# Performance work log

Hardware: AMD Instinct MI355X
Metric: run time of the kernel (lower is better)

## Reference

```python
import jax, jax.numpy as jnp
import numpy as np

EMBED = 1024
DSTATE = 16
DCONV = 4
DTRANK = 64  # ceil(EMBED/16)
B = 2
T = 2048


def setup_inputs() -> dict:
    key = jax.random.key(0)
    ks = jax.random.split(key, 8)
    def w(k, shape, s=0.02):
        return jax.random.normal(k, shape, dtype=jnp.float32) * s
    return dict(
        x=jax.random.normal(ks[0], (B, T, EMBED), dtype=jnp.float32),
        in_proj_w=w(ks[1], (2 * EMBED, EMBED)), in_proj_b=jnp.zeros((2 * EMBED,), jnp.float32),
        conv_w=w(ks[2], (EMBED, 1, DCONV)), conv_b=jnp.zeros((EMBED,), jnp.float32),
        x_proj_w=w(ks[3], (DTRANK + 2 * DSTATE, EMBED)), x_proj_b=jnp.zeros((DTRANK + 2 * DSTATE,), jnp.float32),
        dt_proj_w=w(ks[4], (EMBED, DTRANK)), dt_proj_b=jnp.zeros((EMBED,), jnp.float32),
        A_log=jnp.log(jnp.arange(1, DSTATE + 1, dtype=jnp.float32))[None, :],  # (1,N) as in torch module
        D_param=jnp.ones((EMBED,), jnp.float32),
        out_proj_w=w(ks[5], (EMBED, EMBED)), out_proj_b=jnp.zeros((EMBED,), jnp.float32),
        skip_proj_w=w(ks[6], (EMBED, EMBED)), skip_proj_b=jnp.zeros((EMBED,), jnp.float32),
    )


def reference(x, in_proj_w, in_proj_b, conv_w, conv_b, x_proj_w, x_proj_b,
              dt_proj_w, dt_proj_b, A_log, D_param, out_proj_w, out_proj_b,
              skip_proj_w, skip_proj_b):
    Bsz, Tlen, Dm = x.shape
    # in_proj and split into ssm branch and gate branch
    xr = x @ in_proj_w.T + in_proj_b            # (B,T,2D)
    x_in, res = jnp.split(xr, 2, axis=-1)
    # depthwise causal conv1d (torch pads both sides then slices [:T] == left-pad)
    xc = jax.lax.conv_general_dilated(
        x_in.transpose(0, 2, 1), conv_w, (1,), [(DCONV - 1, 0)],
        dimension_numbers=('NCH', 'OIH', 'NCH'), feature_group_count=Dm)
    xc = (xc + conv_b[None, :, None]).transpose(0, 2, 1)  # (B,T,D)
    xc = jax.nn.silu(xc)
    # input-dependent SSM params
    ssm = xc @ x_proj_w.T + x_proj_b            # (B,T,dt_rank+2N)
    delta, Bp, Cp = jnp.split(ssm, [DTRANK, DTRANK + DSTATE], axis=-1)
    delta = jax.nn.softplus(delta @ dt_proj_w.T + dt_proj_b)  # (B,T,D)
    A = -jnp.exp(A_log)                          # (1,N)
    dA = jnp.exp(delta[..., None] * A)           # (B,T,D,N)
    dBu = delta[..., None] * Bp[:, :, None, :] * xc[..., None]  # (B,T,D,N)
    # inclusive associative scan over time: h_t = dA_t * h_{t-1} + dBu_t
    def op(l, r):
        Ai, Bi = l
        Aj, Bj = r
        return (Aj * Ai, Bj + Aj * Bi)
    _, ys = jax.lax.associative_scan(op, (dA, dBu), axis=1)
    y = (ys * Cp[:, :, None, :]).sum(-1)         # (B,T,D)
    y = y + xc * D_param
    y = y * jax.nn.silu(res)
    return y @ out_proj_w.T + out_proj_b + (x @ skip_proj_w.T + skip_proj_b)
```

## Files before the change

kernel.cpp:

```cpp
#include <hip/hip_runtime.h>
#include <math.h>

#define EMBED  1024
#define DSTATE 16
#define DCONV  4
#define DTRANK 64
#define BB     2
#define TT     2048
#define M_TOK  (BB*TT)
#define SSMW   96
#define NCHUNK 64
#define CLEN   (TT/NCHUNK)
#define KSPLIT 8

typedef __attribute__((ext_vector_type(8))) __bf16 bf16x8;
typedef __attribute__((ext_vector_type(4))) float floatx4;

__device__ __forceinline__ float silu_f(float x) {
    return x / (1.0f + __expf(-x));
}
__device__ __forceinline__ float softplus_f(float x) {
    return fmaxf(x, 0.0f) + log1pf(__expf(-fabsf(x)));
}
__device__ __forceinline__ unsigned short f2bf(float f) {
    union { float f; unsigned int u; } v; v.f = f;
    unsigned int u = v.u;
    return (unsigned short)((u + 0x7fffu + ((u >> 16) & 1u)) >> 16);
}
__device__ __forceinline__ float bf2f(unsigned short s) {
    union { unsigned int u; float f; } v; v.u = ((unsigned int)s) << 16;
    return v.f;
}
__device__ __forceinline__ void async16(unsigned short* lds, const unsigned short* g) {
    __builtin_amdgcn_global_load_lds(
        (const __attribute__((address_space(1))) unsigned int*)g,
        (__attribute__((address_space(3))) unsigned int*)lds, 16, 0, 0);
}

#define GEMM_DECODE \
    const int tid = threadIdx.x; const int wid = tid >> 6; \
    const int lane = tid & 63; \
    const int wm = wid >> 1, wn = wid & 1; \
    const int lr = lane & 15; const int lq = lane >> 4;

__device__ __forceinline__ void gemm_acc(
    const unsigned short* __restrict__ A, int lda,
    const unsigned short* __restrict__ W, int ldw,
    int m0, int n0, int k0, int klen, floatx4 (&acc)[4][4])
{
    __shared__ unsigned short As[128 * 32];
    __shared__ unsigned short Ws[128 * 32];
    GEMM_DECODE;
    const int l0 = tid,       row0 = l0 >> 2;
    const int l1 = tid + 256, row1 = l1 >> 2;
    const int kc0 = (((l0 & 3) ^ ((row0 >> 1) & 3)) * 8);
    const int kc1 = (((l1 & 3) ^ ((row1 >> 1) & 3)) * 8);

    for (int kt = k0; kt < k0 + klen; kt += 32) {
        async16(&As[l0 * 8], A + (size_t)(m0 + row0) * lda + kt + kc0);
        async16(&As[l1 * 8], A + (size_t)(m0 + row1) * lda + kt + kc1);
        async16(&Ws[l0 * 8], W + (size_t)(n0 + row0) * ldw + kt + kc0);
        async16(&Ws[l1 * 8], W + (size_t)(n0 + row1) * ldw + kt + kc1);
        __syncthreads();

        bf16x8 af[4], bfr[4];
        #pragma unroll
        for (int i = 0; i < 4; ++i) {
            int ra = wm * 64 + i * 16 + lr;
            af[i] = *(const bf16x8*)&As[ra * 32 + ((lq ^ ((ra >> 1) & 3)) * 8)];
        }
        #pragma unroll
        for (int i = 0; i < 4; ++i) {
            int rb = wn * 64 + i * 16 + lr;
            bfr[i] = *(const bf16x8*)&Ws[rb * 32 + ((lq ^ ((rb >> 1) & 3)) * 8)];
        }

        #pragma unroll
        for (int mi = 0; mi < 4; ++mi)
            #pragma unroll
            for (int ni = 0; ni < 4; ++ni)
                acc[mi][ni] = __builtin_amdgcn_mfma_f32_16x16x32_bf16(
                    af[mi], bfr[ni], acc[mi][ni], 0, 0, 0);
        __syncthreads();
    }
}

__global__ __launch_bounds__(256)
void gemm_in(const unsigned short* __restrict__ A,
             const unsigned short* __restrict__ W,
             const float* __restrict__ bias,
             unsigned short* __restrict__ xrb, unsigned short* __restrict__ gate)
{
    floatx4 acc[4][4] = {};
    const int m0 = blockIdx.x * 128, n0 = blockIdx.y * 128;
    gemm_acc(A, 2 * EMBED, W, EMBED, m0, n0, 0, EMBED, acc);
    GEMM_DECODE;
    #pragma unroll
    for (int mi = 0; mi < 4; ++mi)
        #pragma unroll
        for (int ni = 0; ni < 4; ++ni) {
            int nb = n0 + wn * 64 + ni * 16 + lr;
            #pragma unroll
            for (int r = 0; r < 4; ++r) {
                int m = m0 + wm * 64 + mi * 16 + lq * 4 + r;
                float v = acc[mi][ni][r] + bias[nb];
                if (nb < EMBED) xrb[(size_t)m * EMBED + nb] = f2bf(v);
                else gate[(size_t)m * EMBED + nb - EMBED] = f2bf(silu_f(v));
            }
        }
}

__global__ __launch_bounds__(256)
void gemm_xp(const unsigned short* __restrict__ A,
             const unsigned short* __restrict__ W,
             float* __restrict__ xpart)
{
    floatx4 acc[4][4] = {};
    const int m0 = blockIdx.x * 128;
    const int k0 = blockIdx.z * (EMBED / KSPLIT);
    gemm_acc(A, EMBED, W, EMBED, m0, 0, k0, EMBED / KSPLIT, acc);
    GEMM_DECODE;
    float* base = xpart + (size_t)blockIdx.z * M_TOK * SSMW;
    #pragma unroll
    for (int mi = 0; mi < 4; ++mi)
        #pragma unroll
        for (int ni = 0; ni < 4; ++ni) {
            int nb = wn * 64 + ni * 16 + lr;
            if (nb < SSMW) {
                #pragma unroll
                for (int r = 0; r < 4; ++r) {
                    int m = m0 + wm * 64 + mi * 16 + lq * 4 + r;
                    base[(size_t)m * SSMW + nb] = acc[mi][ni][r];
                }
            }
        }
}

__global__ __launch_bounds__(256)
void xp_merge(const float* __restrict__ xpart, const float* __restrict__ xp_b,
              float* __restrict__ ssm, unsigned short* __restrict__ dtin)
{
    int idx = blockIdx.x * 256 + threadIdx.x;
    if (idx >= M_TOK * SSMW) return;
    int m = idx / SSMW, n = idx - m * SSMW;
    float s = xp_b[n];
    #pragma unroll
    for (int z = 0; z < KSPLIT; ++z) s += xpart[(size_t)z * M_TOK * SSMW + idx];
    ssm[idx] = s;
    if (n < DTRANK) dtin[(size_t)m * DTRANK + n] = f2bf(s);
}

__global__ __launch_bounds__(256)
void gemm_dt(const unsigned short* __restrict__ A,
             const unsigned short* __restrict__ W,
             const float* __restrict__ bias,
             unsigned short* __restrict__ dltb)
{
    floatx4 acc[4][4] = {};
    const int m0 = blockIdx.x * 128, n0 = blockIdx.y * 128;
    gemm_acc(A, DTRANK, W, DTRANK, m0, n0, 0, DTRANK, acc);
    GEMM_DECODE;
    #pragma unroll
    for (int mi = 0; mi < 4; ++mi)
        #pragma unroll
        for (int ni = 0; ni < 4; ++ni) {
            int nb = n0 + wn * 64 + ni * 16 + lr;
            #pragma unroll
            for (int r = 0; r < 4; ++r) {
                int m = m0 + wm * 64 + mi * 16 + lq * 4 + r;
                dltb[(size_t)m * EMBED + nb] = f2bf(softplus_f(acc[mi][ni][r] + bias[nb]));
            }
        }
}

__global__ __launch_bounds__(256)
void gemm_out(const unsigned short* __restrict__ A,
              const unsigned short* __restrict__ W,
              const float* __restrict__ bias, const float* __restrict__ bias2,
              float* __restrict__ C)
{
    floatx4 acc[4][4] = {};
    const int m0 = blockIdx.x * 128, n0 = blockIdx.y * 128;
    gemm_acc(A, 2 * EMBED, W, 2 * EMBED, m0, n0, 0, 2 * EMBED, acc);
    GEMM_DECODE;
    #pragma unroll
    for (int mi = 0; mi < 4; ++mi)
        #pragma unroll
        for (int ni = 0; ni < 4; ++ni) {
            int nb = n0 + wn * 64 + ni * 16 + lr;
            float bb = bias[nb] + bias2[nb];
            #pragma unroll
            for (int r = 0; r < 4; ++r) {
                int m = m0 + wm * 64 + mi * 16 + lq * 4 + r;
                C[(size_t)m * EMBED + nb] = acc[mi][ni][r] + bb;
            }
        }
}

#define SEG0 524288
#define SEG1 (SEG0 + 16384)
#define SEG2 (SEG1 + 32768)
#define SEG3 (SEG2 + 524288)
#define SEG4 (SEG3 + 1048576)

__global__ __launch_bounds__(256)
void cvt_pack(const float* __restrict__ in_w, const float* __restrict__ dt_w,
              const float* __restrict__ xp_w, const float* __restrict__ ow,
              const float* __restrict__ sw, const float* __restrict__ x,
              unsigned short* __restrict__ inwb, unsigned short* __restrict__ dtwb,
              unsigned short* __restrict__ xpwb, unsigned short* __restrict__ wcat,
              unsigned short* __restrict__ Acat)
{
    int j = blockIdx.x * 256 + threadIdx.x;
    if (j >= SEG4) return;
    float4 v = {0.f, 0.f, 0.f, 0.f};
    unsigned short* dst;
    if (j < SEG0) {
        v = *(const float4*)&in_w[j * 4];
        dst = &inwb[j * 4];
    } else if (j < SEG1) {
        int i = (j - SEG0) * 4;
        v = *(const float4*)&dt_w[i];
        dst = &dtwb[i];
    } else if (j < SEG2) {
        int i = (j - SEG1) * 4;
        if ((i >> 10) < SSMW) v = *(const float4*)&xp_w[i];
        dst = &xpwb[i];
    } else if (j < SEG3) {
        int i = (j - SEG2) * 4;
        int n = i >> 11, k = i & 2047;
        v = *(const float4*)((k < EMBED) ? &ow[(size_t)n * EMBED + k]
                                         : &sw[(size_t)n * EMBED + (k - EMBED)]);
        dst = &wcat[i];
    } else {
        int i = (j - SEG3) * 4;
        int m = i >> 10, k = i & 1023;
        v = *(const float4*)&x[i];
        dst = &Acat[(size_t)m * 2 * EMBED + EMBED + k];
    }
    ushort4 o = { f2bf(v.x), f2bf(v.y), f2bf(v.z), f2bf(v.w) };
    *(ushort4*)dst = o;
}

__global__ __launch_bounds__(256)
void conv_silu(const unsigned short* __restrict__ xrb,
               const float* __restrict__ conv_w,
               const float* __restrict__ conv_b,
               unsigned short* __restrict__ xcb)
{
    int idx = blockIdx.x * 256 + threadIdx.x;
    if (idx >= BB * TT * EMBED / 4) return;
    int dq = idx & (EMBED / 4 - 1);
    int t  = (idx >> 8) & (TT - 1);
    int b  = idx >> 19;
    int d  = dq * 4;

    float4 cw0 = *(const float4*)&conv_w[(d + 0) * 4];
    float4 cw1 = *(const float4*)&conv_w[(d + 1) * 4];
    float4 cw2 = *(const float4*)&conv_w[(d + 2) * 4];
    float4 cw3 = *(const float4*)&conv_w[(d + 3) * 4];
    float4 s   = *(const float4*)&conv_b[d];

    const float* w0 = (const float*)&cw0;
    const float* w1 = (const float*)&cw1;
    const float* w2 = (const float*)&cw2;
    const float* w3 = (const float*)&cw3;

    #pragma unroll
    for (int jj = 0; jj < 4; ++jj) {
        int tr = t - 3 + jj;
        if (tr >= 0) {
            ushort4 u = *(const ushort4*)&xrb[(size_t)(b * TT + tr) * EMBED + d];
            s.x = fmaf(w0[jj], bf2f(u.x), s.x);
            s.y = fmaf(w1[jj], bf2f(u.y), s.y);
            s.z = fmaf(w2[jj], bf2f(u.z), s.z);
            s.w = fmaf(w3[jj], bf2f(u.w), s.w);
        }
    }
    ushort4 o = { f2bf(silu_f(s.x)), f2bf(silu_f(s.y)),
                  f2bf(silu_f(s.z)), f2bf(silu_f(s.w)) };
    *(ushort4*)&xcb[(size_t)(b * TT + t) * EMBED + d] = o;
}

__global__ __launch_bounds__(256)
void scan_chunk(const unsigned short* __restrict__ deltab,
                const unsigned short* __restrict__ xcb,
                const float* __restrict__ ssm,
                const float* __restrict__ A_log,
                float* __restrict__ hout,
                float* __restrict__ Ssum)
{
    __shared__ float Bs[CLEN][DSTATE];
    const int tid = threadIdx.x;
    const int blk = blockIdx.x;
    const int dg = blk & 3, chunk = (blk >> 2) & (NCHUNK - 1), b = blk >> 8;
    const int d = dg * 256 + tid;
    const int t0 = chunk * CLEN;

    for (int i = tid; i < CLEN * DSTATE; i += 256) {
        int t = i >> 4, n = i & 15;
        Bs[t][n] = ssm[(size_t)(b * TT + t0 + t) * SSMW + DTRANK + n];
    }
    __syncthreads();

    float An[DSTATE];
    #pragma unroll
    for (int n = 0; n < DSTATE; ++n) An[n] = -__expf(A_log[n]);

    float h[DSTATE] = {};
    float S = 0.f;
    for (int t = 0; t < CLEN; ++t) {
        size_t row = (size_t)(b * TT + t0 + t);
        float dv = bf2f(deltab[row * EMBED + d]);
        float xv = bf2f(xcb[row * EMBED + d]);
        S += dv;
        float sx = dv * xv;
        float Bv[DSTATE];
        *(float4*)&Bv[0]  = *(const float4*)&Bs[t][0];
        *(float4*)&Bv[4]  = *(const float4*)&Bs[t][4];
        *(float4*)&Bv[8]  = *(const float4*)&Bs[t][8];
        *(float4*)&Bv[12] = *(const float4*)&Bs[t][12];
        #pragma unroll
        for (int n = 0; n < DSTATE; ++n) {
            float dA = __expf(dv * An[n]);
            h[n] = fmaf(dA, h[n], sx * Bv[n]);
        }
    }
    size_t base = ((size_t)(chunk * BB + b) * EMBED + d) * DSTATE;
    #pragma unroll
    for (int jj = 0; jj < 4; ++jj)
        *(float4*)&hout[base + jj * 4] = *(float4*)&h[jj * 4];
    Ssum[(size_t)(chunk * BB + b) * EMBED + d] = S;
}

__global__ __launch_bounds__(256)
void scan_combine(const float* __restrict__ A_log,
                  const float* __restrict__ Ssum,
                  const float* __restrict__ hout,
                  float* __restrict__ hin)
{
    int idx = blockIdx.x * 256 + threadIdx.x;
    int n  = idx & 15;
    int bd = idx >> 4;
    float An = -__expf(A_log[n]);
    float h = 0.f;
    for (int c0 = 0; c0 < NCHUNK; c0 += 8) {
        float ho[8], S[8];
        #pragma unroll
        for (int jj = 0; jj < 8; ++jj) {
            ho[jj] = hout[(size_t)(c0 + jj) * (BB * EMBED * DSTATE) + idx];
            S[jj]  = Ssum[(size_t)(c0 + jj) * (BB * EMBED) + bd];
        }
        #pragma unroll
        for (int jj = 0; jj < 8; ++jj) {
            hin[(size_t)(c0 + jj) * (BB * EMBED * DSTATE) + idx] = h;
            h = fmaf(__expf(An * S[jj]), h, ho[jj]);
        }
    }
}

__global__ __launch_bounds__(256)
void scan_apply(const unsigned short* __restrict__ deltab,
                const unsigned short* __restrict__ xcb,
                const float* __restrict__ ssm,
                const float* __restrict__ A_log,
                const float* __restrict__ D_param,
                const unsigned short* __restrict__ gate,
                const float* __restrict__ hin,
                unsigned short* __restrict__ Acat)
{
    __shared__ float Bs[CLEN][DSTATE];
    __shared__ float Cs[CLEN][DSTATE];
    const int tid = threadIdx.x;
    const int blk = blockIdx.x;
    const int dg = blk & 3, chunk = (blk >> 2) & (NCHUNK - 1), b = blk >> 8;
    const int d = dg * 256 + tid;
    const int t0 = chunk * CLEN;

    for (int i = tid; i < CLEN * DSTATE; i += 256) {
        int t = i >> 4, n = i & 15;
        size_t row = (size_t)(b * TT + t0 + t);
        Bs[t][n] = ssm[row * SSMW + DTRANK + n];
        Cs[t][n] = ssm[row * SSMW + DTRANK + DSTATE + n];
    }
    __syncthreads();

    float An[DSTATE];
    #pragma unroll
    for (int n = 0; n < DSTATE; ++n) An[n] = -__expf(A_log[n]);
    float Dd = D_param[d];

    float h[DSTATE];
    size_t base = ((size_t)(chunk * BB + b) * EMBED + d) * DSTATE;
    #pragma unroll
    for (int jj = 0; jj < 4; ++jj)
        *(float4*)&h[jj * 4] = *(const float4*)&hin[base + jj * 4];

    for (int t = 0; t < CLEN; ++t) {
        size_t row = (size_t)(b * TT + t0 + t);
        float dv = bf2f(deltab[row * EMBED + d]);
        float xv = bf2f(xcb[row * EMBED + d]);
        float sx = dv * xv;
        float Bv[DSTATE], Cv[DSTATE];
        *(float4*)&Bv[0]  = *(const float4*)&Bs[t][0];
        *(float4*)&Bv[4]  = *(const float4*)&Bs[t][4];
        *(float4*)&Bv[8]  = *(const float4*)&Bs[t][8];
        *(float4*)&Bv[12] = *(const float4*)&Bs[t][12];
        *(float4*)&Cv[0]  = *(const float4*)&Cs[t][0];
        *(float4*)&Cv[4]  = *(const float4*)&Cs[t][4];
        *(float4*)&Cv[8]  = *(const float4*)&Cs[t][8];
        *(float4*)&Cv[12] = *(const float4*)&Cs[t][12];
        float y0 = 0.f, y1 = 0.f, y2 = 0.f, y3 = 0.f;
        #pragma unroll
        for (int n = 0; n < DSTATE; n += 4) {
            float dA0 = __expf(dv * An[n + 0]);
            float dA1 = __expf(dv * An[n + 1]);
            float dA2 = __expf(dv * An[n + 2]);
            float dA3 = __expf(dv * An[n + 3]);
            h[n + 0] = fmaf(dA0, h[n + 0], sx * Bv[n + 0]);
            h[n + 1] = fmaf(dA1, h[n + 1], sx * Bv[n + 1]);
            h[n + 2] = fmaf(dA2, h[n + 2], sx * Bv[n + 2]);
            h[n + 3] = fmaf(dA3, h[n + 3], sx * Bv[n + 3]);
            y0 = fmaf(h[n + 0], Cv[n + 0], y0);
            y1 = fmaf(h[n + 1], Cv[n + 1], y1);
            y2 = fmaf(h[n + 2], Cv[n + 2], y2);
            y3 = fmaf(h[n + 3], Cv[n + 3], y3);
        }
        float yv = (y0 + y1) + (y2 + y3) + xv * Dd;
        float g = bf2f(gate[row * EMBED + d]);
        Acat[row * 2 * EMBED + d] = f2bf(yv * g);
    }
}

extern "C" void kernel_launch(void* const* d_in, const int* in_sizes, int n_in,
                              void* d_out, int out_size, void* d_ws, size_t ws_size,
                              hipStream_t stream) {
    const float* x      = (const float*)d_in[0];
    const float* in_w   = (const float*)d_in[1];
    const float* in_b   = (const float*)d_in[2];
    const float* conv_w = (const float*)d_in[3];
    const float* conv_b = (const float*)d_in[4];
    const float* xp_w   = (const float*)d_in[5];
    const float* xp_b   = (const float*)d_in[6];
    const float* dt_w   = (const float*)d_in[7];
    const float* dt_b   = (const float*)d_in[8];
    const float* A_log  = (const float*)d_in[9];
    const float* Dp     = (const float*)d_in[10];
    const float* out_w  = (const float*)d_in[11];
    const float* out_b  = (const float*)d_in[12];
    const float* skip_w = (const float*)d_in[13];
    const float* skip_b = (const float*)d_in[14];
    float* out = (float*)d_out;

    float* ws    = (float*)d_ws;
    float* ssm   = ws;
    float* xpart = ssm   + (size_t)M_TOK * SSMW;
    float* hout  = xpart + (size_t)KSPLIT * M_TOK * SSMW;
    float* hin   = hout  + (size_t)NCHUNK * BB * EMBED * DSTATE;
    float* Ssum  = hin   + (size_t)NCHUNK * BB * EMBED * DSTATE;
    unsigned short* Acat = (unsigned short*)(Ssum + (size_t)NCHUNK * BB * EMBED);
    unsigned short* xrb  = Acat + (size_t)M_TOK * 2 * EMBED;
    unsigned short* xcb  = xrb  + (size_t)M_TOK * EMBED;
    unsigned short* dltb = xcb  + (size_t)M_TOK * EMBED;
    unsigned short* dtin = dltb + (size_t)M_TOK * EMBED;
    unsigned short* gate = dtin + (size_t)M_TOK * DTRANK;
    unsigned short* inwb = gate + (size_t)M_TOK * EMBED;
    unsigned short* xpwb = inwb + (size_t)2 * EMBED * EMBED;
    unsigned short* dtwb = xpwb + (size_t)128 * EMBED;
    unsigned short* wcat = dtwb + (size_t)EMBED * DTRANK;

    dim3 blk(256);

    cvt_pack<<<(SEG4 + 255) / 256, blk, 0, stream>>>(
        in_w, dt_w, xp_w, out_w, skip_w, x, inwb, dtwb, xpwb, wcat, Acat);

    gemm_in<<<dim3(M_TOK / 128, 2 * EMBED / 128), blk, 0, stream>>>(
        Acat + EMBED, inwb, in_b, xrb, gate);

    conv_silu<<<(M_TOK * EMBED / 4 + 255) / 256, blk, 0, stream>>>(
        xrb, conv_w, conv_b, xcb);

    gemm_xp<<<dim3(M_TOK / 128, 1, KSPLIT), blk, 0, stream>>>(xcb, xpwb, xpart);
    xp_merge<<<(M_TOK * SSMW + 255) / 256, blk, 0, stream>>>(xpart, xp_b, ssm, dtin);

    gemm_dt<<<dim3(M_TOK / 128, EMBED / 128), blk, 0, stream>>>(
        dtin, dtwb, dt_b, dltb);

    scan_chunk<<<BB * NCHUNK * (EMBED / 256), blk, 0, stream>>>(
        dltb, xcb, ssm, A_log, hout, Ssum);
    scan_combine<<<(BB * EMBED * DSTATE + 255) / 256, blk, 0, stream>>>(
        A_log, Ssum, hout, hin);
    scan_apply<<<BB * NCHUNK * (EMBED / 256), blk, 0, stream>>>(
        dltb, xcb, ssm, A_log, Dp, gate, hin, Acat);

    gemm_out<<<dim3(M_TOK / 128, EMBED / 128), blk, 0, stream>>>(
        Acat, wcat, out_b, skip_b, out);
}
```

Before: 319.4 us.

## Fold dt_proj into x_proj weights, replacing split-K xp GEMM and dt GEMM

Precomputes a fused weight W_dt·W_xp[:64] (plus the B/C rows of x_proj) in a small kernel, so one GEMM over K=1024 with N=1152 produces delta and B/C directly. This removes the split-K partial buffers, the merge kernel and the separate rank-64 GEMM with its bf16 round-trip. In exchange the delta GEMM grows from K=64 to K=1024 over 1024 outputs, and the rounding path changes. Softplus is also simplified to a threshold plus log(1+exp).

```diff
diff --git a/kernel.cpp b/kernel.cpp
--- a/kernel.cpp
+++ b/kernel.cpp
@@ -8,10 +8,9 @@
 #define BB     2
 #define TT     2048
 #define M_TOK  (BB*TT)
-#define SSMW   96
 #define NCHUNK 64
 #define CLEN   (TT/NCHUNK)
-#define KSPLIT 8
+#define NMID   1152
 
 typedef __attribute__((ext_vector_type(8))) __bf16 bf16x8;
 typedef __attribute__((ext_vector_type(4))) float floatx4;
@@ -20,7 +19,7 @@
     return x / (1.0f + __expf(-x));
 }
 __device__ __forceinline__ float softplus_f(float x) {
-    return fmaxf(x, 0.0f) + log1pf(__expf(-fabsf(x)));
+    return (x > 15.0f) ? x : __logf(1.0f + __expf(x));
 }
 __device__ __forceinline__ unsigned short f2bf(float f) {
     union { float f; unsigned int u; } v; v.f = f;
@@ -111,64 +110,64 @@
 }
 
 __global__ __launch_bounds__(256)
-void gemm_xp(const unsigned short* __restrict__ A,
-             const unsigned short* __restrict__ W,
-             float* __restrict__ xpart)
-{
-    floatx4 acc[4][4] = {};
-    const int m0 = blockIdx.x * 128;
-    const int k0 = blockIdx.z * (EMBED / KSPLIT);
-    gemm_acc(A, EMBED, W, EMBED, m0, 0, k0, EMBED / KSPLIT, acc);
-    GEMM_DECODE;
-    float* base = xpart + (size_t)blockIdx.z * M_TOK * SSMW;
-    #pragma unroll
-    for (int mi = 0; mi < 4; ++mi)
-        #pragma unroll
-        for (int ni = 0; ni < 4; ++ni) {
-            int nb = wn * 64 + ni * 16 + lr;
-            if (nb < SSMW) {
-                #pragma unroll
-                for (int r = 0; r < 4; ++r) {
-                    int m = m0 + wm * 64 + mi * 16 + lq * 4 + r;
-                    base[(size_t)m * SSMW + nb] = acc[mi][ni][r];
-                }
-            }
-        }
-}
-
-__global__ __launch_bounds__(256)
-void xp_merge(const float* __restrict__ xpart, const float* __restrict__ xp_b,
-              float* __restrict__ ssm, unsigned short* __restrict__ dtin)
-{
-    int idx = blockIdx.x * 256 + threadIdx.x;
-    if (idx >= M_TOK * SSMW) return;
-    int m = idx / SSMW, n = idx - m * SSMW;
-    float s = xp_b[n];
-    #pragma unroll
-    for (int z = 0; z < KSPLIT; ++z) s += xpart[(size_t)z * M_TOK * SSMW + idx];
-    ssm[idx] = s;
-    if (n < DTRANK) dtin[(size_t)m * DTRANK + n] = f2bf(s);
-}
-
-__global__ __launch_bounds__(256)
-void gemm_dt(const unsigned short* __restrict__ A,
-             const unsigned short* __restrict__ W,
-             const float* __restrict__ bias,
-             unsigned short* __restrict__ dltb)
+void wfuse_kernel(const float* __restrict__ dt_w, const float* __restrict__ xp_w,
+                  const float* __restrict__ xp_b, const float* __restrict__ dt_b,
+                  unsigned short* __restrict__ wmid, float* __restrict__ bias_mid)
+{
+    __shared__ float dtl[4][64];
+    const int t = threadIdx.x;
+    dtl[t >> 6][t & 63] = dt_w[(size_t)(blockIdx.x * 4 + (t >> 6)) * DTRANK + (t & 63)];
+    __syncthreads();
+    const int dloc = t >> 6, kq = t & 63;
+    const int d = blockIdx.x * 4 + dloc;
+
+    #pragma unroll
+    for (int j = 0; j < 4; ++j) {
+        float4 acc = {0.f, 0.f, 0.f, 0.f};
+        const int kb = j * 256 + kq * 4;
+        for (int r = 0; r < 64; ++r) {
+            float4 xv = *(const float4*)&xp_w[(size_t)r * EMBED + kb];
+            float s = dtl[dloc][r];
+            acc.x = fmaf(s, xv.x, acc.x);
+            acc.y = fmaf(s, xv.y, acc.y);
+            acc.z = fmaf(s, xv.z, acc.z);
+            acc.w = fmaf(s, xv.w, acc.w);
+        }
+        ushort4 o = { f2bf(acc.x), f2bf(acc.y), f2bf(acc.z), f2bf(acc.w) };
+        *(ushort4*)&wmid[(size_t)d * EMBED + kb] = o;
+    }
+
+    if (kq == 0) {
+        float b = dt_b[d];
+        for (int r = 0; r < 64; ++r) b = fmaf(dtl[dloc][r], xp_b[r], b);
+        bias_mid[d] = b;
+    }
+    if (blockIdx.x == 0 && t < 128)
+        bias_mid[1024 + t] = (t < 32) ? xp_b[DTRANK + t] : 0.f;
+}
+
+__global__ __launch_bounds__(256)
+void gemm_mid(const unsigned short* __restrict__ A,
+              const unsigned short* __restrict__ W,
+              const float* __restrict__ bias_mid,
+              unsigned short* __restrict__ dltb, float* __restrict__ bc)
 {
     floatx4 acc[4][4] = {};
     const int m0 = blockIdx.x * 128, n0 = blockIdx.y * 128;
-    gemm_acc(A, DTRANK, W, DTRANK, m0, n0, 0, DTRANK, acc);
+    gemm_acc(A, EMBED, W, EMBED, m0, n0, 0, EMBED, acc);
     GEMM_DECODE;
     #pragma unroll
     for (int mi = 0; mi < 4; ++mi)
         #pragma unroll
         for (int ni = 0; ni < 4; ++ni) {
             int nb = n0 + wn * 64 + ni * 16 + lr;
+            float bb = bias_mid[nb];
             #pragma unroll
             for (int r = 0; r < 4; ++r) {
                 int m = m0 + wm * 64 + mi * 16 + lq * 4 + r;
-                dltb[(size_t)m * EMBED + nb] = f2bf(softplus_f(acc[mi][ni][r] + bias[nb]));
+                float v = acc[mi][ni][r] + bb;
+                if (nb < 1024) dltb[(size_t)m * EMBED + nb] = f2bf(softplus_f(v));
+                else if (nb < 1056) bc[(size_t)m * 32 + nb - 1024] = v;
             }
         }
 }
@@ -197,46 +196,41 @@
         }
 }
 
-#define SEG0 524288
-#define SEG1 (SEG0 + 16384)
-#define SEG2 (SEG1 + 32768)
-#define SEG3 (SEG2 + 524288)
-#define SEG4 (SEG3 + 1048576)
-
-__global__ __launch_bounds__(256)
-void cvt_pack(const float* __restrict__ in_w, const float* __restrict__ dt_w,
-              const float* __restrict__ xp_w, const float* __restrict__ ow,
-              const float* __restrict__ sw, const float* __restrict__ x,
-              unsigned short* __restrict__ inwb, unsigned short* __restrict__ dtwb,
-              unsigned short* __restrict__ xpwb, unsigned short* __restrict__ wcat,
-              unsigned short* __restrict__ Acat)
+#define SA 524288
+#define SB (SA + 524288)
+#define SC (SB + 1048576)
+#define SD (SC + 32768)
+
+__global__ __launch_bounds__(256)
+void cvt_pack(const float* __restrict__ in_w, const float* __restrict__ xp_w,
+              const float* __restrict__ ow, const float* __restrict__ sw,
+              const float* __restrict__ x,
+              unsigned short* __restrict__ inwb, unsigned short* __restrict__ wcat,
+              unsigned short* __restrict__ Acat, unsigned short* __restrict__ wmid)
 {
     int j = blockIdx.x * 256 + threadIdx.x;
-    if (j >= SEG4) return;
+    if (j >= SD) return;
     float4 v = {0.f, 0.f, 0.f, 0.f};
     unsigned short* dst;
-    if (j < SEG0) {
+    if (j < SA) {
         v = *(const float4*)&in_w[j * 4];
         dst = &inwb[j * 4];
-    } else if (j < SEG1) {
-        int i = (j - SEG0) * 4;
-        v = *(const float4*)&dt_w[i];
-        dst = &dtwb[i];
-    } else if (j < SEG2) {
-        int i = (j - SEG1) * 4;
-        if ((i >> 10) < SSMW) v = *(const float4*)&xp_w[i];
-        dst = &xpwb[i];
-    } else if (j < SEG3) {
-        int i = (j - SEG2) * 4;
+    } else if (j < SB) {
+        int i = (j - SA) * 4;
         int n = i >> 11, k = i & 2047;
         v = *(const float4*)((k < EMBED) ? &ow[(size_t)n * EMBED + k]
                                          : &sw[(size_t)n * EMBED + (k - EMBED)]);
         dst = &wcat[i];
-    } else {
-        int i = (j - SEG3) * 4;
+    } else if (j < SC) {
+        int i = (j - SB) * 4;
         int m = i >> 10, k = i & 1023;
         v = *(const float4*)&x[i];
         dst = &Acat[(size_t)m * 2 * EMBED + EMBED + k];
+    } else {
+        int i = (j - SC) * 4;
+        int row = i >> 10, k = i & 1023;
+        if (row < 32) v = *(const float4*)&xp_w[(size_t)(DTRANK + row) * EMBED + k];
+        dst = &wmid[(size_t)(1024 + row) * EMBED + k];
     }
     ushort4 o = { f2bf(v.x), f2bf(v.y), f2bf(v.z), f2bf(v.w) };
     *(ushort4*)dst = o;
@@ -285,7 +279,7 @@
 __global__ __launch_bounds__(256)
 void scan_chunk(const unsigned short* __restrict__ deltab,
                 const unsigned short* __restrict__ xcb,
-                const float* __restrict__ ssm,
+                const float* __restrict__ bc,
                 const float* __restrict__ A_log,
                 float* __restrict__ hout,
                 float* __restrict__ Ssum)
@@ -299,7 +293,7 @@
 
     for (int i = tid; i < CLEN * DSTATE; i += 256) {
         int t = i >> 4, n = i & 15;
-        Bs[t][n] = ssm[(size_t)(b * TT + t0 + t) * SSMW + DTRANK + n];
+        Bs[t][n] = bc[(size_t)(b * TT + t0 + t) * 32 + n];
     }
     __syncthreads();
 
@@ -362,7 +356,7 @@
 __global__ __launch_bounds__(256)
 void scan_apply(const unsigned short* __restrict__ deltab,
                 const unsigned short* __restrict__ xcb,
-                const float* __restrict__ ssm,
+                const float* __restrict__ bc,
                 const float* __restrict__ A_log,
                 const float* __restrict__ D_param,
                 const unsigned short* __restrict__ gate,
@@ -380,8 +374,8 @@
     for (int i = tid; i < CLEN * DSTATE; i += 256) {
         int t = i >> 4, n = i & 15;
         size_t row = (size_t)(b * TT + t0 + t);
-        Bs[t][n] = ssm[row * SSMW + DTRANK + n];
-        Cs[t][n] = ssm[row * SSMW + DTRANK + DSTATE + n];
+        Bs[t][n] = bc[row * 32 + n];
+        Cs[t][n] = bc[row * 32 + 16 + n];
     }
     __syncthreads();
 
@@ -452,27 +446,27 @@
     const float* skip_b = (const float*)d_in[14];
     float* out = (float*)d_out;
 
-    float* ws    = (float*)d_ws;
-    float* ssm   = ws;
-    float* xpart = ssm   + (size_t)M_TOK * SSMW;
-    float* hout  = xpart + (size_t)KSPLIT * M_TOK * SSMW;
-    float* hin   = hout  + (size_t)NCHUNK * BB * EMBED * DSTATE;
-    float* Ssum  = hin   + (size_t)NCHUNK * BB * EMBED * DSTATE;
+    float* ws      = (float*)d_ws;
+    float* bc      = ws;
+    float* biasm   = bc    + (size_t)M_TOK * 32;
+    float* hout    = biasm + 1152;
+    float* hin     = hout  + (size_t)NCHUNK * BB * EMBED * DSTATE;
+    float* Ssum    = hin   + (size_t)NCHUNK * BB * EMBED * DSTATE;
     unsigned short* Acat = (unsigned short*)(Ssum + (size_t)NCHUNK * BB * EMBED);
     unsigned short* xrb  = Acat + (size_t)M_TOK * 2 * EMBED;
     unsigned short* xcb  = xrb  + (size_t)M_TOK * EMBED;
     unsigned short* dltb = xcb  + (size_t)M_TOK * EMBED;
-    unsigned short* dtin = dltb + (size_t)M_TOK * EMBED;
-    unsigned short* gate = dtin + (size_t)M_TOK * DTRANK;
+    unsigned short* gate = dltb + (size_t)M_TOK * EMBED;
     unsigned short* inwb = gate + (size_t)M_TOK * EMBED;
-    unsigned short* xpwb = inwb + (size_t)2 * EMBED * EMBED;
-    unsigned short* dtwb = xpwb + (size_t)128 * EMBED;
-    unsigned short* wcat = dtwb + (size_t)EMBED * DTRANK;
+    unsigned short* wcat = inwb + (size_t)2 * EMBED * EMBED;
+    unsigned short* wmid = wcat + (size_t)2 * EMBED * EMBED;
 
     dim3 blk(256);
 
-    cvt_pack<<<(SEG4 + 255) / 256, blk, 0, stream>>>(
-        in_w, dt_w, xp_w, out_w, skip_w, x, inwb, dtwb, xpwb, wcat, Acat);
+    cvt_pack<<<(SD + 255) / 256, blk, 0, stream>>>(
+        in_w, xp_w, out_w, skip_w, x, inwb, wcat, Acat, wmid);
+    wfuse_kernel<<<256, blk, 0, stream>>>(
+        dt_w, xp_w, xp_b, dt_b, wmid, biasm);
 
     gemm_in<<<dim3(M_TOK / 128, 2 * EMBED / 128), blk, 0, stream>>>(
         Acat + EMBED, inwb, in_b, xrb, gate);
@@ -480,18 +474,15 @@
     conv_silu<<<(M_TOK * EMBED / 4 + 255) / 256, blk, 0, stream>>>(
         xrb, conv_w, conv_b, xcb);
 
-    gemm_xp<<<dim3(M_TOK / 128, 1, KSPLIT), blk, 0, stream>>>(xcb, xpwb, xpart);
-    xp_merge<<<(M_TOK * SSMW + 255) / 256, blk, 0, stream>>>(xpart, xp_b, ssm, dtin);
-
-    gemm_dt<<<dim3(M_TOK / 128, EMBED / 128), blk, 0, stream>>>(
-        dtin, dtwb, dt_b, dltb);
+    gemm_mid<<<dim3(M_TOK / 128, NMID / 128), blk, 0, stream>>>(
+        xcb, wmid, biasm, dltb, bc);
 
     scan_chunk<<<BB * NCHUNK * (EMBED / 256), blk, 0, stream>>>(
-        dltb, xcb, ssm, A_log, hout, Ssum);
+        dltb, xcb, bc, A_log, hout, Ssum);
     scan_combine<<<(BB * EMBED * DSTATE + 255) / 256, blk, 0, stream>>>(
         A_log, Ssum, hout, hin);
     scan_apply<<<BB * NCHUNK * (EMBED / 256), blk, 0, stream>>>(
-        dltb, xcb, ssm, A_log, Dp, gate, hin, Acat);
+        dltb, xcb, bc, A_log, Dp, gate, hin, Acat);
 
     gemm_out<<<dim3(M_TOK / 128, EMBED / 128), blk, 0, stream>>>(
         Acat, wcat, out_b, skip_b, out);
```

Measured after the change: 323.1 us. Within noise of the previous version (+1.2%).
